# Optimization experiments

Hardware: AMD Instinct MI355X
Metric: run time of the kernel (lower is better)

The kernel has to match this reference:

```python
import jax, jax.numpy as jnp
import numpy as np

B, S, D = 2, 2048, 1024
H, DK, DV = 16, 64, 64


def setup_inputs() -> dict:
    key = jax.random.key(0)
    ks = jax.random.split(key, 9)
    s = 0.02
    return {
        "x": jax.random.normal(ks[0], (B, S, D), dtype=jnp.float32),
        "mask": jnp.zeros((B, S), dtype=bool),  # True = padded position
        "Wq": jax.random.normal(ks[1], (D, H * DK), dtype=jnp.float32) * s,
        "bq": jnp.zeros((H * DK,), dtype=jnp.float32),
        "Wk": jax.random.normal(ks[2], (D, H * DK), dtype=jnp.float32) * s,
        "bk": jnp.zeros((H * DK,), dtype=jnp.float32),
        "Wv": jax.random.normal(ks[3], (D, H * DV), dtype=jnp.float32) * s,
        "bv": jnp.zeros((H * DV,), dtype=jnp.float32),
        "Wo": jax.random.normal(ks[4], (H * DV, D), dtype=jnp.float32) * s,
        "bo": jnp.zeros((D,), dtype=jnp.float32),
    }


def reference(x, mask, Wq, bq, Wk, bk, Wv, bv, Wo, bo):
    Bx, Sx, _ = x.shape
    # projections -> [B, H, S, dk/dv]
    q = (x @ Wq + bq).reshape(Bx, Sx, H, DK).transpose(0, 2, 1, 3)
    k = (x @ Wk + bk).reshape(Bx, Sx, H, DK).transpose(0, 2, 1, 3)
    v = (x @ Wv + bv).reshape(Bx, Sx, H, DV).transpose(0, 2, 1, 3)
    # scaled QK^T: [B, H, Sq, Sk]
    scores = jnp.einsum("bhqd,bhkd->bhqk", q, k) / jnp.sqrt(jnp.float32(DK))
    neg_inf = jnp.float32(-jnp.inf)
    # padding mask: True masks out key positions
    scores = jnp.where(mask[:, None, None, :], neg_inf, scores)
    # causal mask
    causal = jnp.triu(jnp.ones((Sx, Sx), dtype=bool), k=1)
    scores = jnp.where(causal[None, None, :, :], neg_inf, scores)
    attn = jax.nn.softmax(scores, axis=-1)
    out = jnp.einsum("bhqk,bhkd->bhqd", attn, v)  # [B, H, S, dv]
    out = out.transpose(0, 2, 1, 3).reshape(Bx, Sx, H * DV)
    return out @ Wo + bo
```

## Files before the change

### kernel.cpp

```cpp
#include <hip/hip_runtime.h>
#include <stdint.h>

typedef __bf16 bf16_t;
typedef __bf16 bf16x8 __attribute__((ext_vector_type(8)));
typedef float f32x4 __attribute__((ext_vector_type(4)));

#define S_LEN 2048
#define D_MODEL 1024
#define NH 16
#define DKV 64
#define BATCH 2

#define QSCALE 0.1803368801111204f

__device__ __forceinline__ uint16_t f2bfu(float f) {
    union { float f; uint32_t u; } c; c.f = f;
    return (uint16_t)((c.u + 0x7fffu + ((c.u >> 16) & 1u)) >> 16);
}
__device__ __forceinline__ bf16_t f2bf(float f) {
    union { uint16_t s; bf16_t b; } o; o.s = f2bfu(f);
    return o.b;
}
__device__ __forceinline__ uint32_t pack2t(float lo, float hi) {
    union { float f; uint32_t u; } a, b; a.f = lo; b.f = hi;
    return __builtin_amdgcn_perm(b.u, a.u, 0x07060302);
}
__device__ __forceinline__ uint32_t pack2r(float lo, float hi) {
    union { float f; uint32_t u; } a, b; a.f = lo; b.f = hi;
    uint32_t alo = a.u + 0x7fffu + ((a.u >> 16) & 1u);
    uint32_t bhi = b.u + 0x7fffu + ((b.u >> 16) & 1u);
    return __builtin_amdgcn_perm(bhi, alo, 0x07060302);
}
__device__ __forceinline__ float exp2_native(float x) {
    float r;
    asm("v_exp_f32 %0, %1" : "=v"(r) : "v"(x));
    return r;
}
__device__ __forceinline__ void gld_lds16(const bf16_t* g, bf16_t* l) {
    __builtin_amdgcn_global_load_lds(
        (const __attribute__((address_space(1))) void*)g,
        (__attribute__((address_space(3))) void*)l, 16, 0, 0);
}

__global__ __launch_bounds__(256) void k_prep(
    const float* __restrict__ x, bf16_t* __restrict__ xb,
    const float* __restrict__ Wq, const float* __restrict__ Wk,
    const float* __restrict__ Wv, const float* __restrict__ Wo,
    bf16_t* __restrict__ WqkvT, bf16_t* __restrict__ WoT) {
    __shared__ float tile[64][65];
    int bid = blockIdx.x;
    if (bid < 4096) {
        int i = (bid * 256 + threadIdx.x) * 4;
        float4 v = *(const float4*)(x + i);
        xb[i + 0] = f2bf(v.x);
        xb[i + 1] = f2bf(v.y);
        xb[i + 2] = f2bf(v.z);
        xb[i + 3] = f2bf(v.w);
        return;
    }
    int b2 = bid - 4096;
    int k0 = (b2 & 15) * 64;
    int n0 = (b2 >> 4) * 64;
    const float* W; bf16_t* WT; int np, nw;
    if (n0 < 3072) {
        W = (n0 < 1024) ? Wq : (n0 < 2048) ? Wk : Wv;
        np = n0 & 1023; WT = WqkvT; nw = n0;
    } else {
        W = Wo; np = n0 - 3072; WT = WoT; nw = n0 - 3072;
    }
    int tx = threadIdx.x & 63, ty = threadIdx.x >> 6;
    #pragma unroll
    for (int r = ty; r < 64; r += 4)
        tile[r][tx] = W[(size_t)(k0 + r) * 1024 + np + tx];
    __syncthreads();
    #pragma unroll
    for (int r = ty; r < 64; r += 4)
        WT[(size_t)(nw + r) * 1024 + k0 + tx] = f2bf(tile[tx][r]);
}

#define BM 128
#define BN 128

__global__ __launch_bounds__(256) void k_gemm_qkv(
    const bf16_t* __restrict__ A, const bf16_t* __restrict__ BT, int K,
    const float* __restrict__ bias0, const float* __restrict__ bias1,
    const float* __restrict__ bias2,
    bf16_t* __restrict__ outQ, bf16_t* __restrict__ outK, bf16_t* __restrict__ outVt) {
    __shared__ __align__(16) bf16_t smem[4 * 128 * 32];
    bf16_t* const As0 = smem;
    bf16_t* const As1 = smem + 128 * 32;
    bf16_t* const Bs0 = smem + 2 * 128 * 32;
    bf16_t* const Bs1 = smem + 3 * 128 * 32;
    int m0 = blockIdx.x * BM;
    int n0 = blockIdx.y * BN;
    int t = threadIdx.x;
    int wid = t >> 6, lane = t & 63, l15 = lane & 15, quad = lane >> 4;
    int wr = (wid >> 1) * 64, wc = (wid & 1) * 64;
    int sr = t >> 2;
    int sc = (t & 3) ^ ((sr >> 1) & 3);
    int sl = (t & 3) * 8;
    const f32x4 fzero = {0.f, 0.f, 0.f, 0.f};
    f32x4 acc[4][4];
    #pragma unroll
    for (int i = 0; i < 4; i++)
        #pragma unroll
        for (int j = 0; j < 4; j++) acc[i][j] = fzero;

    int secb = n0 >> 10;
    int colA = (quad ^ ((l15 >> 1) & 3)) << 3;

    auto STAGE = [&](bf16_t* __restrict__ Ad, bf16_t* __restrict__ Bd, int k0) {
        #pragma unroll
        for (int p = 0; p < 2; p++) {
            int r = p * 64 + sr;
            gld_lds16(&A[(size_t)(m0 + r) * K + k0 + sc * 8], &Ad[r * 32 + sl]);
            gld_lds16(&BT[(size_t)(n0 + r) * K + k0 + sc * 8], &Bd[r * 32 + sl]);
        }
    };

    auto STEP = [&](const bf16_t* __restrict__ Ar, const bf16_t* __restrict__ Br,
                    bf16_t* __restrict__ Aw, bf16_t* __restrict__ Bw, int i) {
        if (i + 1 < 32) STAGE(Aw, Bw, (i + 1) * 32);
        bf16x8 af[4], bfr[4];
        #pragma unroll
        for (int mt = 0; mt < 4; mt++)
            af[mt] = *(const bf16x8*)&Ar[(wr + mt * 16 + l15) * 32 + colA];
        #pragma unroll
        for (int nt = 0; nt < 4; nt++)
            bfr[nt] = *(const bf16x8*)&Br[(wc + nt * 16 + l15) * 32 + colA];
        __builtin_amdgcn_s_setprio(1);
        if (secb == 2) {
            #pragma unroll
            for (int mt = 0; mt < 4; mt++)
                #pragma unroll
                for (int nt = 0; nt < 4; nt++)
                    acc[mt][nt] = __builtin_amdgcn_mfma_f32_16x16x32_bf16(
                        af[mt], bfr[nt], acc[mt][nt], 0, 0, 0);
        } else {
            #pragma unroll
            for (int i2 = 0; i2 < 4; i2++)
                #pragma unroll
                for (int j = 0; j < 4; j++)
                    acc[i2][j] = __builtin_amdgcn_mfma_f32_16x16x32_bf16(
                        bfr[i2], af[j], acc[i2][j], 0, 0, 0);
        }
        __builtin_amdgcn_s_setprio(0);
        if (i + 1 < 32) __syncthreads();
    };

    STAGE(As0, Bs0, 0);
    __syncthreads();
    for (int i = 0; i < 32; i += 2) {
        STEP(As0, Bs0, As1, Bs1, i);
        STEP(As1, Bs1, As0, Bs0, i + 1);
    }

    if (secb == 2) {
        __syncthreads();
        bf16_t* const Ct = smem;
        int nbase = n0 & 1023;
        #pragma unroll
        for (int mt = 0; mt < 4; mt++) {
            #pragma unroll
            for (int nt = 0; nt < 4; nt++) {
                int dl = wc + nt * 16 + l15;
                float bv = bias2[nbase + dl];
                int sl2 = wr + mt * 16 + quad * 4;
                uint2 pk;
                pk.x = pack2t(acc[mt][nt][0] + bv, acc[mt][nt][1] + bv);
                pk.y = pack2t(acc[mt][nt][2] + bv, acc[mt][nt][3] + bv);
                int c4 = (sl2 >> 2) ^ ((dl & 7) << 1);
                *(uint2*)&Ct[dl * 128 + c4 * 4] = pk;
            }
        }
        __syncthreads();
        int b = m0 >> 11, sb = m0 & 2047;
        #pragma unroll
        for (int rr = 0; rr < 8; rr++) {
            int row = rr * 16 + (t >> 4);
            int s8 = t & 15;
            int c4 = (s8 * 2) ^ ((row & 7) << 1);
            uint4 vv = *(const uint4*)&Ct[row * 128 + c4 * 4];
            int nn = nbase + row;
            int h = nn >> 6, d = nn & 63;
            *(uint4*)&outVt[(((size_t)(b * NH + h)) * DKV + d) * S_LEN + sb + s8 * 8] = vv;
        }
        return;
    }

    {
        const float* bias = (secb == 0) ? bias0 : bias1;
        bf16_t* outP = (secb == 0) ? outQ : outK;
        float scale = (secb == 0) ? QSCALE : 1.0f;
        #pragma unroll
        for (int i = 0; i < 4; i++) {
            #pragma unroll
            for (int j = 0; j < 4; j++) {
                int nn = (n0 + wc + i * 16 + quad * 4) & 1023;
                float4 bv = *(const float4*)&bias[nn];
                int gr = m0 + wr + j * 16 + l15;
                int b = gr >> 11, s = gr & 2047;
                int h = nn >> 6, d0 = nn & 63;
                float v0 = (acc[i][j][0] + bv.x) * scale;
                float v1 = (acc[i][j][1] + bv.y) * scale;
                float v2 = (acc[i][j][2] + bv.z) * scale;
                float v3 = (acc[i][j][3] + bv.w) * scale;
                uint2 pk;
                pk.x = pack2r(v0, v1);
                pk.y = pack2r(v2, v3);
                *(uint2*)&outP[(((size_t)(b * NH + h)) * S_LEN + s) * DKV + d0] = pk;
            }
        }
    }
}

__global__ __launch_bounds__(256) void k_gemm_out(
    const bf16_t* __restrict__ A, const bf16_t* __restrict__ BT, int N, int K,
    const float* __restrict__ bias, float* __restrict__ outF) {
    __shared__ __align__(16) bf16_t As0[128 * 32];
    __shared__ __align__(16) bf16_t As1[128 * 32];
    __shared__ __align__(16) bf16_t Bs0[64 * 32];
    __shared__ __align__(16) bf16_t Bs1[64 * 32];
    int m0 = blockIdx.x * 128;
    int n0 = blockIdx.y * 64;
    int t = threadIdx.x;
    int wid = t >> 6, lane = t & 63, l15 = lane & 15, quad = lane >> 4;
    int wr = wid * 32;
    int sr = t >> 2;
    int sc = (t & 3) ^ ((sr >> 1) & 3);
    int sl = (t & 3) * 8;
    const f32x4 fzero = {0.f, 0.f, 0.f, 0.f};
    f32x4 acc[4][2];
    #pragma unroll
    for (int i = 0; i < 4; i++)
        #pragma unroll
        for (int j = 0; j < 2; j++) acc[i][j] = fzero;

    int colA = (quad ^ ((l15 >> 1) & 3)) << 3;

    auto STAGE = [&](bf16_t* __restrict__ Ad, bf16_t* __restrict__ Bd, int k0) {
        #pragma unroll
        for (int p = 0; p < 2; p++) {
            int r = p * 64 + sr;
            gld_lds16(&A[(size_t)(m0 + r) * K + k0 + sc * 8], &Ad[r * 32 + sl]);
        }
        gld_lds16(&BT[(size_t)(n0 + sr) * K + k0 + sc * 8], &Bd[sr * 32 + sl]);
    };

    auto STEP = [&](const bf16_t* __restrict__ Ar, const bf16_t* __restrict__ Br,
                    bf16_t* __restrict__ Aw, bf16_t* __restrict__ Bw, int i) {
        if (i + 1 < 32) STAGE(Aw, Bw, (i + 1) * 32);
        bf16x8 af[2], bfr[4];
        #pragma unroll
        for (int j = 0; j < 2; j++)
            af[j] = *(const bf16x8*)&Ar[(wr + j * 16 + l15) * 32 + colA];
        #pragma unroll
        for (int i2 = 0; i2 < 4; i2++)
            bfr[i2] = *(const bf16x8*)&Br[(i2 * 16 + l15) * 32 + colA];
        __builtin_amdgcn_s_setprio(1);
        #pragma unroll
        for (int i2 = 0; i2 < 4; i2++)
            #pragma unroll
            for (int j = 0; j < 2; j++)
                acc[i2][j] = __builtin_amdgcn_mfma_f32_16x16x32_bf16(
                    bfr[i2], af[j], acc[i2][j], 0, 0, 0);
        __builtin_amdgcn_s_setprio(0);
        if (i + 1 < 32) __syncthreads();
    };

    STAGE(As0, Bs0, 0);
    __syncthreads();
    for (int i = 0; i < 32; i += 2) {
        STEP(As0, Bs0, As1, Bs1, i);
        STEP(As1, Bs1, As0, Bs0, i + 1);
    }

    #pragma unroll
    for (int i = 0; i < 4; i++) {
        #pragma unroll
        for (int j = 0; j < 2; j++) {
            int nc = n0 + i * 16 + quad * 4;
            float4 bv = *(const float4*)&bias[nc];
            int mr = m0 + wr + j * 16 + l15;
            float4 o;
            o.x = acc[i][j][0] + bv.x;
            o.y = acc[i][j][1] + bv.y;
            o.z = acc[i][j][2] + bv.z;
            o.w = acc[i][j][3] + bv.w;
            *(float4*)&outF[(size_t)mr * N + nc] = o;
        }
    }
}

__global__ __launch_bounds__(256, 4) void k_attn11(
    const bf16_t* __restrict__ Q, const bf16_t* __restrict__ Kg,
    const bf16_t* __restrict__ Vt, const unsigned char* __restrict__ mask,
    bf16_t* __restrict__ O) {
    __shared__ __align__(16) bf16_t Ks0[64 * 64];
    __shared__ __align__(16) bf16_t Ks1[64 * 64];
    __shared__ __align__(16) bf16_t Vs0[64 * 64];
    __shared__ __align__(16) bf16_t Vs1[64 * 64];
    __shared__ __align__(16) bf16_t Ps[64 * 64];

    int bid = blockIdx.x;
    int bh = bid & 31;
    int u = bid >> 5;
    int a = u & 7, g2 = u >> 3;
    int qt = (g2 == 0) ? 31 - a : (g2 == 1) ? a : (g2 == 2) ? 23 - a : 8 + a;
    int b = bh >> 4, h = bh & 15;
    int t = threadIdx.x;
    int w = t >> 6, lane = t & 63, l15 = lane & 15, quad = lane >> 4;
    int r7 = l15 & 7;

    bool maskany;
    {
        const uint2* mrow = (const uint2*)&mask[b * S_LEN];
        uint2 m0 = mrow[lane], m1 = mrow[lane + 64];
        uint2 m2 = mrow[lane + 128], m3 = mrow[lane + 192];
        uint32_t mo = (m0.x | m0.y) | (m1.x | m1.y) | (m2.x | m2.y) | (m3.x | m3.y);
        maskany = __any(mo != 0);
    }

    const bf16_t* Qrow = Q + ((size_t)bh * S_LEN + qt * 64 + w * 16 + l15) * DKV;
    bf16x8 qf0 = *(const bf16x8*)&Qrow[quad * 8];
    bf16x8 qf1 = *(const bf16x8*)&Qrow[32 + quad * 8];

    const bf16_t* Kbh = Kg + (size_t)bh * S_LEN * DKV;
    const bf16_t* Vbh = Vt + (size_t)bh * DKV * S_LEN;

    const f32x4 fzero = {0.f, 0.f, 0.f, 0.f};
    f32x4 oacc[4];
    f32x4 lacc = fzero;
    #pragma unroll
    for (int nt = 0; nt < 4; nt++) oacc[nt] = fzero;

    const bf16_t one_b = (bf16_t)1.0f;
    const bf16x8 onesf = {one_b, one_b, one_b, one_b, one_b, one_b, one_b, one_b};

    int qg = qt * 64 + w * 16 + l15;
    int qmin = qt * 64 + w * 16;

    int sr = t >> 3;
    int sc = (t & 7) ^ (sr & 7);
    int sl = (t & 7) * 8;

    #pragma unroll
    for (int p = 0; p < 2; p++) {
        int r = p * 32 + sr;
        gld_lds16(&Kbh[(size_t)r * DKV + sc * 8], &Ks0[r * 64 + sl]);
        gld_lds16(&Vbh[(size_t)r * S_LEN + sc * 8], &Vs0[r * 64 + sl]);
    }
    __syncthreads();

    auto TILE = [&](const bf16_t* __restrict__ Kr, const bf16_t* __restrict__ Vr,
                    bf16_t* __restrict__ Kw, bf16_t* __restrict__ Vw, int kt) {
        if (kt < qt) {
            int kb2 = (kt + 1) * 64;
            #pragma unroll
            for (int p = 0; p < 2; p++) {
                int r = p * 32 + sr;
                gld_lds16(&Kbh[(size_t)(kb2 + r) * DKV + sc * 8], &Kw[r * 64 + sl]);
                gld_lds16(&Vbh[(size_t)r * S_LEN + kb2 + sc * 8], &Vw[r * 64 + sl]);
            }
        }
        int kbase = kt * 64;

        f32x4 sacc[4];
        #pragma unroll
        for (int mt = 0; mt < 4; mt++) sacc[mt] = fzero;
        #pragma unroll
        for (int kk = 0; kk < 64; kk += 32) {
            bf16x8 qf = kk ? qf1 : qf0;
            int col = (((quad + (kk >> 3)) ^ r7) << 3);
            bf16x8 af[4];
            #pragma unroll
            for (int mt = 0; mt < 4; mt++)
                af[mt] = *(const bf16x8*)&Kr[(mt * 16 + l15) * 64 + col];
            __builtin_amdgcn_s_setprio(1);
            #pragma unroll
            for (int mt = 0; mt < 4; mt++)
                sacc[mt] = __builtin_amdgcn_mfma_f32_16x16x32_bf16(af[mt], qf, sacc[mt], 0, 0, 0);
            __builtin_amdgcn_s_setprio(0);
        }

        if (maskany) {
            #pragma unroll
            for (int mt = 0; mt < 4; mt++) {
                uint32_t mb = *(const uint32_t*)&mask[b * S_LEN + kbase + mt * 16 + quad * 4];
                #pragma unroll
                for (int r = 0; r < 4; r++)
                    sacc[mt][r] += (float)((mb >> (8 * r)) & 0xffu) * -1e30f;
            }
        }
        if (kt == qt) {
            #pragma unroll
            for (int mt = 0; mt < 4; mt++) {
                int kgb = kbase + mt * 16 + quad * 4;
                #pragma unroll
                for (int r = 0; r < 4; r++)
                    if (kgb + r > qg) sacc[mt][r] = -1e30f;
            }
        }
        #pragma unroll
        for (int mt = 0; mt < 4; mt++) {
            uint2 pk;
            pk.x = pack2t(exp2_native(sacc[mt][0]), exp2_native(sacc[mt][1]));
            pk.y = pack2t(exp2_native(sacc[mt][2]), exp2_native(sacc[mt][3]));
            int pc = (mt * 2 + (quad >> 1)) ^ r7;
            *(uint2*)&Ps[(w * 16 + l15) * 64 + pc * 8 + (quad & 1) * 4] = pk;
        }

        #pragma unroll
        for (int kk = 0; kk < 64; kk += 32) {
            int vcol = (((quad + (kk >> 3)) ^ r7) << 3);
            bf16x8 pf = *(const bf16x8*)&Ps[(w * 16 + l15) * 64 + vcol];
            bf16x8 vf[4];
            #pragma unroll
            for (int nt = 0; nt < 4; nt++)
                vf[nt] = *(const bf16x8*)&Vr[(nt * 16 + l15) * 64 + vcol];
            __builtin_amdgcn_s_setprio(1);
            #pragma unroll
            for (int nt = 0; nt < 4; nt++)
                oacc[nt] = __builtin_amdgcn_mfma_f32_16x16x32_bf16(pf, vf[nt], oacc[nt], 0, 0, 0);
            lacc = __builtin_amdgcn_mfma_f32_16x16x32_bf16(pf, onesf, lacc, 0, 0, 0);
            __builtin_amdgcn_s_setprio(0);
        }

        if (kt < qt) __syncthreads();
    };

    for (int kt = 0; kt <= qt; kt += 2) {
        TILE(Ks0, Vs0, Ks1, Vs1, kt);
        if (kt + 1 <= qt) TILE(Ks1, Vs1, Ks0, Vs0, kt + 1);
    }

    #pragma unroll
    for (int r = 0; r < 4; r++) {
        float l = lacc[r];
        float invl = l > 0.f ? 1.f / l : 0.f;
        int q = qt * 64 + w * 16 + quad * 4 + r;
        #pragma unroll
        for (int nt = 0; nt < 4; nt++) {
            int d = nt * 16 + l15;
            O[((size_t)b * S_LEN + q) * D_MODEL + h * DKV + d] = f2bf(oacc[nt][r] * invl);
        }
    }
}

extern "C" void kernel_launch(void* const* d_in, const int* in_sizes, int n_in,
                              void* d_out, int out_size, void* d_ws, size_t ws_size,
                              hipStream_t stream) {
    const float* x = (const float*)d_in[0];
    const unsigned char* mask = (const unsigned char*)d_in[1];
    const float* Wq = (const float*)d_in[2];
    const float* bq = (const float*)d_in[3];
    const float* Wk = (const float*)d_in[4];
    const float* bk = (const float*)d_in[5];
    const float* Wv = (const float*)d_in[6];
    const float* bv = (const float*)d_in[7];
    const float* Wo = (const float*)d_in[8];
    const float* bo = (const float*)d_in[9];
    float* out = (float*)d_out;

    char* ws = (char*)d_ws;
    const size_t MB = 1024 * 1024;
    bf16_t* xb    = (bf16_t*)(ws + 0 * MB);
    bf16_t* WqkvT = (bf16_t*)(ws + 8 * MB);
    bf16_t* WoT   = (bf16_t*)(ws + 14 * MB);
    bf16_t* Qb    = (bf16_t*)(ws + 16 * MB);
    bf16_t* Kb    = (bf16_t*)(ws + 24 * MB);
    bf16_t* Vtb   = (bf16_t*)(ws + 32 * MB);
    bf16_t* AOb   = (bf16_t*)(ws + 40 * MB);

    k_prep<<<dim3(4096 + 1024), dim3(256), 0, stream>>>(
        x, xb, Wq, Wk, Wv, Wo, WqkvT, WoT);
    k_gemm_qkv<<<dim3(32, 24), dim3(256), 0, stream>>>(
        xb, WqkvT, 1024, bq, bk, bv, Qb, Kb, Vtb);
    k_attn11<<<dim3(1024), dim3(256), 0, stream>>>(Qb, Kb, Vtb, mask, AOb);
    k_gemm_out<<<dim3(32, 16), dim3(256), 0, stream>>>(
        AOb, WoT, 1024, 1024, bo, out);
}
```

Before: 174.6 us.

## Halve attention key tile to 32 and skip fully masked per-warp subtiles

The attention kernel now streams K/V in 32-key tiles instead of 64, which halves shared memory per block and raises the launch-bounds occupancy target from 4 to 6 blocks. Each warp skips the QK, softmax and PV work for subtiles that lie entirely above its causal diagonal, and causal masking is applied only where a subtile crosses the diagonal. The cost is twice as many loop iterations and block barriers, plus a new swizzle layout for V and P.

```diff
diff --git a/kernel.cpp b/kernel.cpp
--- a/kernel.cpp
+++ b/kernel.cpp
@@ -292,15 +292,15 @@
     }
 }
 
-__global__ __launch_bounds__(256, 4) void k_attn11(
+__global__ __launch_bounds__(256, 6) void k_attn13(
     const bf16_t* __restrict__ Q, const bf16_t* __restrict__ Kg,
     const bf16_t* __restrict__ Vt, const unsigned char* __restrict__ mask,
     bf16_t* __restrict__ O) {
-    __shared__ __align__(16) bf16_t Ks0[64 * 64];
-    __shared__ __align__(16) bf16_t Ks1[64 * 64];
-    __shared__ __align__(16) bf16_t Vs0[64 * 64];
-    __shared__ __align__(16) bf16_t Vs1[64 * 64];
-    __shared__ __align__(16) bf16_t Ps[64 * 64];
+    __shared__ __align__(16) bf16_t Ks0[32 * 64];
+    __shared__ __align__(16) bf16_t Ks1[32 * 64];
+    __shared__ __align__(16) bf16_t Vs0[64 * 32];
+    __shared__ __align__(16) bf16_t Vs1[64 * 32];
+    __shared__ __align__(16) bf16_t Ps[64 * 32];
 
     int bid = blockIdx.x;
     int bh = bid & 31;
@@ -311,6 +311,7 @@
     int t = threadIdx.x;
     int w = t >> 6, lane = t & 63, l15 = lane & 15, quad = lane >> 4;
     int r7 = l15 & 7;
+    int k3 = (l15 >> 1) & 3;
 
     bool maskany;
     {
@@ -337,87 +338,79 @@
     const bf16_t one_b = (bf16_t)1.0f;
     const bf16x8 onesf = {one_b, one_b, one_b, one_b, one_b, one_b, one_b, one_b};
 
-    int qg = qt * 64 + w * 16 + l15;
     int qmin = qt * 64 + w * 16;
-
-    int sr = t >> 3;
-    int sc = (t & 7) ^ (sr & 7);
-    int sl = (t & 7) * 8;
-
-    #pragma unroll
-    for (int p = 0; p < 2; p++) {
-        int r = p * 32 + sr;
-        gld_lds16(&Kbh[(size_t)r * DKV + sc * 8], &Ks0[r * 64 + sl]);
-        gld_lds16(&Vbh[(size_t)r * S_LEN + sc * 8], &Vs0[r * 64 + sl]);
-    }
+    int qmax = qmin + 15;
+    int qg = qmin + l15;
+
+    int srK = t >> 3;
+    int scK = (t & 7) ^ (srK & 7);
+    int slK = (t & 7) * 8;
+    int srV = t >> 2;
+    int scV = (t & 3) ^ ((srV >> 1) & 3);
+    int slV = (t & 3) * 8;
+
+    gld_lds16(&Kbh[(size_t)srK * DKV + scK * 8], &Ks0[srK * 64 + slK]);
+    gld_lds16(&Vbh[(size_t)srV * S_LEN + scV * 8], &Vs0[srV * 32 + slV]);
     __syncthreads();
+
+    int ktmax = 2 * qt + 1;
 
     auto TILE = [&](const bf16_t* __restrict__ Kr, const bf16_t* __restrict__ Vr,
                     bf16_t* __restrict__ Kw, bf16_t* __restrict__ Vw, int kt) {
-        if (kt < qt) {
-            int kb2 = (kt + 1) * 64;
-            #pragma unroll
-            for (int p = 0; p < 2; p++) {
-                int r = p * 32 + sr;
-                gld_lds16(&Kbh[(size_t)(kb2 + r) * DKV + sc * 8], &Kw[r * 64 + sl]);
-                gld_lds16(&Vbh[(size_t)r * S_LEN + kb2 + sc * 8], &Vw[r * 64 + sl]);
-            }
-        }
-        int kbase = kt * 64;
-
-        f32x4 sacc[4];
-        #pragma unroll
-        for (int mt = 0; mt < 4; mt++) sacc[mt] = fzero;
-        #pragma unroll
-        for (int kk = 0; kk < 64; kk += 32) {
-            bf16x8 qf = kk ? qf1 : qf0;
-            int col = (((quad + (kk >> 3)) ^ r7) << 3);
-            bf16x8 af[4];
-            #pragma unroll
-            for (int mt = 0; mt < 4; mt++)
-                af[mt] = *(const bf16x8*)&Kr[(mt * 16 + l15) * 64 + col];
-            __builtin_amdgcn_s_setprio(1);
-            #pragma unroll
-            for (int mt = 0; mt < 4; mt++)
-                sacc[mt] = __builtin_amdgcn_mfma_f32_16x16x32_bf16(af[mt], qf, sacc[mt], 0, 0, 0);
-            __builtin_amdgcn_s_setprio(0);
-        }
-
-        if (maskany) {
-            #pragma unroll
-            for (int mt = 0; mt < 4; mt++) {
-                uint32_t mb = *(const uint32_t*)&mask[b * S_LEN + kbase + mt * 16 + quad * 4];
+        if (kt < ktmax) {
+            int kb2 = (kt + 1) * 32;
+            gld_lds16(&Kbh[(size_t)(kb2 + srK) * DKV + scK * 8], &Kw[srK * 64 + slK]);
+            gld_lds16(&Vbh[(size_t)srV * S_LEN + kb2 + scV * 8], &Vw[srV * 32 + slV]);
+        }
+        int kbase = kt * 32;
+        if (kbase <= qmax) {
+            f32x4 sacc[2];
+            sacc[0] = fzero; sacc[1] = fzero;
+            #pragma unroll
+            for (int kk = 0; kk < 64; kk += 32) {
+                bf16x8 qf = kk ? qf1 : qf0;
+                int col = (((quad + (kk >> 3)) ^ r7) << 3);
+                bf16x8 af0 = *(const bf16x8*)&Kr[l15 * 64 + col];
+                bf16x8 af1 = *(const bf16x8*)&Kr[(16 + l15) * 64 + col];
+                __builtin_amdgcn_s_setprio(1);
+                sacc[0] = __builtin_amdgcn_mfma_f32_16x16x32_bf16(af0, qf, sacc[0], 0, 0, 0);
+                sacc[1] = __builtin_amdgcn_mfma_f32_16x16x32_bf16(af1, qf, sacc[1], 0, 0, 0);
+                __builtin_amdgcn_s_setprio(0);
+            }
+
+            if (maskany) {
                 #pragma unroll
-                for (int r = 0; r < 4; r++)
-                    sacc[mt][r] += (float)((mb >> (8 * r)) & 0xffu) * -1e30f;
-            }
-        }
-        if (kt == qt) {
-            #pragma unroll
-            for (int mt = 0; mt < 4; mt++) {
-                int kgb = kbase + mt * 16 + quad * 4;
+                for (int mt = 0; mt < 2; mt++) {
+                    uint32_t mb = *(const uint32_t*)&mask[b * S_LEN + kbase + mt * 16 + quad * 4];
+                    #pragma unroll
+                    for (int r = 0; r < 4; r++)
+                        sacc[mt][r] += (float)((mb >> (8 * r)) & 0xffu) * -1e30f;
+                }
+            }
+            if (kbase + 31 > qmin) {
                 #pragma unroll
-                for (int r = 0; r < 4; r++)
-                    if (kgb + r > qg) sacc[mt][r] = -1e30f;
-            }
-        }
-        #pragma unroll
-        for (int mt = 0; mt < 4; mt++) {
-            uint2 pk;
-            pk.x = pack2t(exp2_native(sacc[mt][0]), exp2_native(sacc[mt][1]));
-            pk.y = pack2t(exp2_native(sacc[mt][2]), exp2_native(sacc[mt][3]));
-            int pc = (mt * 2 + (quad >> 1)) ^ r7;
-            *(uint2*)&Ps[(w * 16 + l15) * 64 + pc * 8 + (quad & 1) * 4] = pk;
-        }
-
-        #pragma unroll
-        for (int kk = 0; kk < 64; kk += 32) {
-            int vcol = (((quad + (kk >> 3)) ^ r7) << 3);
-            bf16x8 pf = *(const bf16x8*)&Ps[(w * 16 + l15) * 64 + vcol];
+                for (int mt = 0; mt < 2; mt++) {
+                    int kgb = kbase + mt * 16 + quad * 4;
+                    #pragma unroll
+                    for (int r = 0; r < 4; r++)
+                        if (kgb + r > qg) sacc[mt][r] = -1e30f;
+                }
+            }
+            #pragma unroll
+            for (int mt = 0; mt < 2; mt++) {
+                uint2 pk;
+                pk.x = pack2t(exp2_native(sacc[mt][0]), exp2_native(sacc[mt][1]));
+                pk.y = pack2t(exp2_native(sacc[mt][2]), exp2_native(sacc[mt][3]));
+                int c4 = (mt * 2 + (quad >> 1)) ^ k3;
+                *(uint2*)&Ps[(w * 16 + l15) * 32 + c4 * 8 + (quad & 1) * 4] = pk;
+            }
+
+            int vcol = (quad ^ k3) << 3;
+            bf16x8 pf = *(const bf16x8*)&Ps[(w * 16 + l15) * 32 + vcol];
             bf16x8 vf[4];
             #pragma unroll
             for (int nt = 0; nt < 4; nt++)
-                vf[nt] = *(const bf16x8*)&Vr[(nt * 16 + l15) * 64 + vcol];
+                vf[nt] = *(const bf16x8*)&Vr[(nt * 16 + l15) * 32 + vcol];
             __builtin_amdgcn_s_setprio(1);
             #pragma unroll
             for (int nt = 0; nt < 4; nt++)
@@ -425,13 +418,12 @@
             lacc = __builtin_amdgcn_mfma_f32_16x16x32_bf16(pf, onesf, lacc, 0, 0, 0);
             __builtin_amdgcn_s_setprio(0);
         }
-
-        if (kt < qt) __syncthreads();
+        if (kt < ktmax) __syncthreads();
     };
 
-    for (int kt = 0; kt <= qt; kt += 2) {
+    for (int kt = 0; kt <= ktmax; kt += 2) {
         TILE(Ks0, Vs0, Ks1, Vs1, kt);
-        if (kt + 1 <= qt) TILE(Ks1, Vs1, Ks0, Vs0, kt + 1);
+        TILE(Ks1, Vs1, Ks0, Vs0, kt + 1);
     }
 
     #pragma unroll
@@ -476,7 +468,7 @@
         x, xb, Wq, Wk, Wv, Wo, WqkvT, WoT);
     k_gemm_qkv<<<dim3(32, 24), dim3(256), 0, stream>>>(
         xb, WqkvT, 1024, bq, bk, bv, Qb, Kb, Vtb);
-    k_attn11<<<dim3(1024), dim3(256), 0, stream>>>(Qb, Kb, Vtb, mask, AOb);
+    k_attn13<<<dim3(1024), dim3(256), 0, stream>>>(Qb, Kb, Vtb, mask, AOb);
     k_gemm_out<<<dim3(32, 16), dim3(256), 0, stream>>>(
         AOb, WoT, 1024, 1024, bo, out);
 }
```

Result: slower. 187.9 us (+7.6%).
